# Kernel tuning notes

Hardware: AMD Instinct MI355X
Metric: run time of the kernel (lower is better)

The kernel has to match this reference:

```python
import jax, jax.numpy as jnp
import numpy as np

C = 512
B, H, W = 4, 64, 64
GROUPS = 32
EPS = 1e-6
SCALE = 1.0 / np.sqrt(C)


def setup_inputs() -> dict:
    key = jax.random.key(0)
    ks = jax.random.split(key, 3)
    x = jax.random.normal(ks[0], (B, C, H, W), dtype=jnp.float32)
    # conv weights: kaiming-ish small init for numerical sanity
    qkv_w = jax.random.normal(ks[1], (3 * C, C), dtype=jnp.float32) * (1.0 / np.sqrt(C))
    proj_w = jax.random.normal(ks[2], (C, C), dtype=jnp.float32) * (1.0 / np.sqrt(C))
    return {
        "x": x,
        "norm_w": jnp.ones((C,), jnp.float32),
        "norm_b": jnp.zeros((C,), jnp.float32),
        "qkv_w": qkv_w,
        "qkv_b": jnp.zeros((3 * C,), jnp.float32),
        "proj_w": proj_w,
        "proj_b": jnp.zeros((C,), jnp.float32),
    }


def reference(x, norm_w, norm_b, qkv_w, qkv_b, proj_w, proj_b):
    b, c, h, w = x.shape
    hw = h * w
    # GroupNorm(32, eps=1e-6, affine)
    xg = x.reshape(b, GROUPS, -1)                       # [B, G, (C/G)*H*W]
    mean = jnp.mean(xg, axis=-1, keepdims=True)
    var = jnp.var(xg, axis=-1, keepdims=True)
    xn = ((xg - mean) * jax.lax.rsqrt(var + EPS)).reshape(b, c, h, w)
    xn = xn * norm_w[:, None, None] + norm_b[:, None, None]
    # 1x1 conv qkv == channel matmul
    qkv = jnp.einsum('oc,bchw->bohw', qkv_w, xn) + qkv_b[:, None, None]
    q, k, v = jnp.split(qkv, 3, axis=1)                 # each [B, C, H, W]
    q = q.reshape(b, c, hw)                              # [B, C, HW]
    k = k.reshape(b, c, hw)
    v = v.reshape(b, c, hw)
    # attn[b, i, j] = softmax_j( q_i . k_j * scale )
    scores = jnp.einsum('bci,bcj->bij', q, k) * SCALE    # [B, HW, HW]
    attn = jax.nn.softmax(scores, axis=-1)
    # h[b, c, i] = sum_j v[b, c, j] * attn[b, i, j]
    hmap = jnp.einsum('bcj,bij->bci', v, attn).reshape(b, c, h, w)
    out = x + jnp.einsum('oc,bchw->bohw', proj_w, hmap) + proj_b[:, None, None]
    return out
```

## Files before the change

### kernel.cpp

```cpp
#include <hip/hip_runtime.h>
#include <hip/hip_fp8.h>
#include <cstdint>
#include <cmath>

#define B_   4
#define C_   512
#define HW_  4096
#define G_   32
#define CPG_ 16
#define EPS_ 1e-6f
#define SCALE_ 0.04419417382415922f
#define PSCALE_ 0.0625f


typedef __bf16 bf16_t;
typedef __bf16 bf16x8 __attribute__((ext_vector_type(8)));
typedef float  f32x4  __attribute__((ext_vector_type(4)));
typedef int    i32x4  __attribute__((ext_vector_type(4)));
typedef int    i32x8  __attribute__((ext_vector_type(8)));
typedef unsigned int u32;
typedef __hip_fp8_e4m3 fp8_t;

__device__ __forceinline__ void cp16(const void* g, void* l) {
  __builtin_amdgcn_global_load_lds((__attribute__((address_space(1))) u32*)(g),
                                   (__attribute__((address_space(3))) u32*)(l),
                                   16, 0, 0);
}

__device__ __forceinline__ void zero_acc(f32x4 acc[4][4]) {
  f32x4 z = {0.f, 0.f, 0.f, 0.f};
#pragma unroll
  for (int i = 0; i < 4; ++i)
#pragma unroll
    for (int j = 0; j < 4; ++j) acc[i][j] = z;
}

template <bool ROWSUM, int SA = 0x7F, int SB = 0x7F>
__device__ __forceinline__ void gemm_bt_mx(const unsigned char* __restrict__ A,
                                           const unsigned char* __restrict__ B,
                                           int K, int lda, int ldb,
                                           f32x4 acc[4][4], f32x4 accl[4]) {
  __shared__ __align__(16) unsigned char As[2][128 * 128];
  __shared__ __align__(16) unsigned char Bs[2][128 * 128];
  const int tid  = threadIdx.x;
  const int wave = tid >> 6;
  const int lane = tid & 63;
  const int wm = (wave >> 1) * 64;
  const int wn = (wave & 1) * 64;
  const int srow = lane >> 3;
  const int gch  = ((lane & 7) - srow) & 7;
  const unsigned char* gA = A + (size_t)(wave * 32 + srow) * lda + gch * 16;
  const unsigned char* gB = B + (size_t)(wave * 32 + srow) * ldb + gch * 16;
  const int lofs = wave * 32 * 128;
  const int fr = lane & 15;
  const int q  = lane >> 4;
  const int co0 = ((2 * q     + fr) & 7) * 16;
  const int co1 = ((2 * q + 1 + fr) & 7) * 16;
  const i32x8 vones = {0x38383838, 0x38383838, 0x38383838, 0x38383838,
                       0x38383838, 0x38383838, 0x38383838, 0x38383838};

  const int nT = K >> 7;
#pragma unroll
  for (int cc = 0; cc < 4; ++cc) {
    cp16(gA + (size_t)(cc * 8) * lda, &As[0][lofs + cc * 1024]);
    cp16(gB + (size_t)(cc * 8) * ldb, &Bs[0][lofs + cc * 1024]);
  }
  gA += 128; gB += 128;

#pragma unroll 1
  for (int t = 0; t < nT; ++t) {
    const int cur = t & 1;
    if (t + 1 < nT) {
#pragma unroll
      for (int cc = 0; cc < 4; ++cc) {
        cp16(gA + (size_t)(cc * 8) * lda, &As[cur ^ 1][lofs + cc * 1024]);
        cp16(gB + (size_t)(cc * 8) * ldb, &Bs[cur ^ 1][lofs + cc * 1024]);
      }
      gA += 128; gB += 128;
      asm volatile("s_waitcnt vmcnt(8)" ::: "memory");
    } else {
      asm volatile("s_waitcnt vmcnt(0)" ::: "memory");
    }
    __builtin_amdgcn_s_barrier();

    i32x8 a[4], b[4];
    const unsigned char* Ab = As[cur];
    const unsigned char* Bb = Bs[cur];
#pragma unroll
    for (int i = 0; i < 4; ++i) {
      const int ro = (wm + i * 16 + fr) * 128;
      i32x4 lo = *(const i32x4*)(Ab + ro + co0);
      i32x4 hi = *(const i32x4*)(Ab + ro + co1);
      a[i] = __builtin_shufflevector(lo, hi, 0, 1, 2, 3, 4, 5, 6, 7);
    }
#pragma unroll
    for (int j = 0; j < 4; ++j) {
      const int ro = (wn + j * 16 + fr) * 128;
      i32x4 lo = *(const i32x4*)(Bb + ro + co0);
      i32x4 hi = *(const i32x4*)(Bb + ro + co1);
      b[j] = __builtin_shufflevector(lo, hi, 0, 1, 2, 3, 4, 5, 6, 7);
    }
    __builtin_amdgcn_s_setprio(1);
#pragma unroll
    for (int i = 0; i < 4; ++i) {
#pragma unroll
      for (int j = 0; j < 4; ++j)
        acc[i][j] = __builtin_amdgcn_mfma_scale_f32_16x16x128_f8f6f4(
            a[i], b[j], acc[i][j], 0, 0, 0, SA, 0, SB);
      if (ROWSUM)
        accl[i] = __builtin_amdgcn_mfma_scale_f32_16x16x128_f8f6f4(
            a[i], vones, accl[i], 0, 0, 0, SA, 0, 0x7F);
    }
    __builtin_amdgcn_s_setprio(0);
    __builtin_amdgcn_s_barrier();
  }
}


__global__ void __launch_bounds__(256) cast_w_kernel(const float* __restrict__ qkv_w,
                                                     const float* __restrict__ proj_w,
                                                     fp8_t* __restrict__ wqkv8,
                                                     fp8_t* __restrict__ wproj8) {
  const int idx = blockIdx.x * 256 + threadIdx.x;
  const int t = idx * 4;
  const int nq = 1536 * 512;
  if (t < nq) {
    u32 dw = 0;
    dw = (u32)__builtin_amdgcn_cvt_pk_fp8_f32(qkv_w[t] * 16.f, qkv_w[t + 1] * 16.f, (int)dw, false);
    dw = (u32)__builtin_amdgcn_cvt_pk_fp8_f32(qkv_w[t + 2] * 16.f, qkv_w[t + 3] * 16.f, (int)dw, true);
    *(u32*)((unsigned char*)wqkv8 + t) = dw;
  } else {
    const int tt = t - nq;
    const int o = tt >> 9;
    const int p = tt & 511;
    float v[4];
#pragma unroll
    for (int e = 0; e < 4; ++e) {
      const int pe = p + e;
      const int off = pe & 63;
      const int c = (pe & ~63) + ((off & 3) << 4) + (off >> 2);
      v[e] = proj_w[(o << 9) + c] * 16.f;
    }
    u32 dw = 0;
    dw = (u32)__builtin_amdgcn_cvt_pk_fp8_f32(v[0], v[1], (int)dw, false);
    dw = (u32)__builtin_amdgcn_cvt_pk_fp8_f32(v[2], v[3], (int)dw, true);
    *(u32*)((unsigned char*)wproj8 + tt) = dw;
  }
}

__global__ void __launch_bounds__(256) gn_partial_kernel(const float* __restrict__ x,
                                                         float* __restrict__ stats) {
  __shared__ float rs[256], rss[256];
  const int bg = blockIdx.x >> 3;
  const int ch = blockIdx.x & 7;
  const float4* base = (const float4*)(x + (size_t)bg * (CPG_ * HW_)) +
                       (size_t)ch * (CPG_ * HW_ / 4 / 8);
  float s = 0.f, ss = 0.f;
  for (int i = threadIdx.x; i < CPG_ * HW_ / 4 / 8; i += 256) {
    float4 v = base[i];
    s  += v.x + v.y + v.z + v.w;
    ss += v.x * v.x + v.y * v.y + v.z * v.z + v.w * v.w;
  }
  rs[threadIdx.x] = s; rss[threadIdx.x] = ss;
  __syncthreads();
  for (int st = 128; st > 0; st >>= 1) {
    if ((int)threadIdx.x < st) {
      rs[threadIdx.x]  += rs[threadIdx.x + st];
      rss[threadIdx.x] += rss[threadIdx.x + st];
    }
    __syncthreads();
  }
  if (threadIdx.x == 0) {
    atomicAdd(&stats[bg * 2 + 0], rs[0]);
    atomicAdd(&stats[bg * 2 + 1], rss[0]);
  }
}

__global__ void __launch_bounds__(256) norm_tr_kernel(const float* __restrict__ x,
                                                      const float* __restrict__ stats,
                                                      const float* __restrict__ nw,
                                                      const float* __restrict__ nb,
                                                      fp8_t* __restrict__ xnT8) {
  __shared__ float tile[64][65];
  const int b  = blockIdx.z;
  const int i0 = blockIdx.x * 64;
  const int c0 = blockIdx.y * 64;
  const int tx = threadIdx.x & 63;
  const int ty = threadIdx.x >> 6;
  const int cbase = c0 + ty * 16;
  const int g = cbase >> 4;
  const float inv = 1.f / (float)(CPG_ * HW_);
  const float sum  = stats[(b * G_ + g) * 2 + 0];
  const float ssum = stats[(b * G_ + g) * 2 + 1];
  const float mean = sum * inv;
  const float rstd = rsqrtf(ssum * inv - mean * mean + EPS_);
#pragma unroll
  for (int r = 0; r < 16; ++r) {
    const int c = cbase + r;
    float v = x[((size_t)b * C_ + c) * HW_ + i0 + tx];
    tile[ty * 16 + r][tx] = (v - mean) * rstd * nw[c] + nb[c];
  }
  __syncthreads();
  const int il = threadIdx.x >> 2;
  const int q4 = threadIdx.x & 3;
#pragma unroll
  for (int m = 0; m < 4; ++m) {
    const int cq = q4 + m * 4;
    u32 dw = 0;
    dw = (u32)__builtin_amdgcn_cvt_pk_fp8_f32(tile[cq * 4 + 0][il], tile[cq * 4 + 1][il], (int)dw, false);
    dw = (u32)__builtin_amdgcn_cvt_pk_fp8_f32(tile[cq * 4 + 2][il], tile[cq * 4 + 3][il], (int)dw, true);
    *(u32*)((unsigned char*)xnT8 + ((size_t)b * HW_ + i0 + il) * C_ + c0 + cq * 4) = dw;
  }
}


__global__ void __launch_bounds__(256) qk_gemm_kernel(const fp8_t* __restrict__ xnT8,
                                                      const fp8_t* __restrict__ wqkv8,
                                                      const float* __restrict__ qkv_b,
                                                      fp8_t* __restrict__ QKt8) {
  const int b = blockIdx.z;
  f32x4 acc[4][4]; zero_acc(acc);
  const unsigned char* A  = (const unsigned char*)xnT8 + ((size_t)b * HW_ + blockIdx.y * 128) * C_;
  const unsigned char* Bp = (const unsigned char*)wqkv8 + (size_t)blockIdx.x * 128 * C_;
  gemm_bt_mx<false, 0x7F, 0x7B>(A, Bp, C_, C_, C_, acc, nullptr);
  const int lane = threadIdx.x & 63, wave = threadIdx.x >> 6;
  const int wm = (wave >> 1) * 64, wn = (wave & 1) * 64;
  const int fr = lane & 15, q = lane >> 4;
  const int r0 = blockIdx.y * 128 + wm + (q << 2);
  const int cb = blockIdx.x * 128 + wn;
  float bias[4];
#pragma unroll
  for (int j = 0; j < 4; ++j) bias[j] = qkv_b[cb + fr + j * 16];
#pragma unroll
  for (int i = 0; i < 4; ++i)
#pragma unroll
    for (int r = 0; r < 4; ++r) {
      const int row = r0 + i * 16 + r;
      u32 dw = 0;
      dw = (u32)__builtin_amdgcn_cvt_pk_fp8_f32(acc[i][0][r] + bias[0],
                                                acc[i][1][r] + bias[1], (int)dw, false);
      dw = (u32)__builtin_amdgcn_cvt_pk_fp8_f32(acc[i][2][r] + bias[2],
                                                acc[i][3][r] + bias[3], (int)dw, true);
      *(u32*)((unsigned char*)QKt8 + ((size_t)b * HW_ + row) * 1024 + cb + fr * 4) = dw;
    }
}

__global__ void __launch_bounds__(256) v_gemm_kernel(const fp8_t* __restrict__ wqkv8,
                                                     const fp8_t* __restrict__ xnT8,
                                                     const float* __restrict__ qkv_b,
                                                     fp8_t* __restrict__ V8) {
  const int b = blockIdx.z;
  f32x4 acc[4][4]; zero_acc(acc);
  const unsigned char* A  = (const unsigned char*)wqkv8 + (size_t)(1024 + blockIdx.y * 128) * C_;
  const unsigned char* Bp = (const unsigned char*)xnT8 + ((size_t)b * HW_ + blockIdx.x * 128) * C_;
  gemm_bt_mx<false, 0x7B, 0x7F>(A, Bp, C_, C_, C_, acc, nullptr);
  const int lane = threadIdx.x & 63, wave = threadIdx.x >> 6;
  const int wm = (wave >> 1) * 64, wn = (wave & 1) * 64;
  const int fr = lane & 15, q = lane >> 4;
  const int r0 = blockIdx.y * 128 + wm + (q << 2);
  const int cb = blockIdx.x * 128 + wn;
#pragma unroll
  for (int i = 0; i < 4; ++i)
#pragma unroll
    for (int r = 0; r < 4; ++r) {
      const int row = r0 + i * 16 + r;
      const float bias = qkv_b[1024 + row];
      u32 dw = 0;
      dw = (u32)__builtin_amdgcn_cvt_pk_fp8_f32(acc[i][0][r] + bias,
                                                acc[i][1][r] + bias, (int)dw, false);
      dw = (u32)__builtin_amdgcn_cvt_pk_fp8_f32(acc[i][2][r] + bias,
                                                acc[i][3][r] + bias, (int)dw, true);
      *(u32*)((unsigned char*)V8 + ((size_t)b * C_ + row) * HW_ + cb + fr * 4) = dw;
    }
}

__global__ void __launch_bounds__(256) sexp_gemm_kernel(const fp8_t* __restrict__ QKt8,
                                                        fp8_t* __restrict__ P8) {
  const int n   = blockIdx.x;
  const int xcd = n & 7;
  const int p   = n >> 3;
  const int xb  = p & 31;
  const int grp = xcd * 16 + (p >> 5);
  const int yb  = grp & 31;
  const int b   = grp >> 5;

  const unsigned char* QKtb = (const unsigned char*)QKt8 + (size_t)b * HW_ * 1024;
  fp8_t* Pb = P8 + (size_t)b * HW_ * HW_;
  f32x4 acc[4][4]; zero_acc(acc);
  const unsigned char* A  = QKtb + (size_t)yb * 128 * 1024;
  const unsigned char* Bp = QKtb + 512 + (size_t)xb * 128 * 1024;
  gemm_bt_mx<false>(A, Bp, 512, 1024, 1024, acc, nullptr);
  const int lane = threadIdx.x & 63, wave = threadIdx.x >> 6;
  const int wm = (wave >> 1) * 64, wn = (wave & 1) * 64;
  const int fr = lane & 15, q = lane >> 4;
  const int r0 = yb * 128 + wm + (q << 2);
  const int cb = xb * 128 + wn;
#pragma unroll
  for (int i = 0; i < 4; ++i)
#pragma unroll
    for (int r = 0; r < 4; ++r) {
      const int row = r0 + i * 16 + r;
      float e0 = __expf(acc[i][0][r] * SCALE_) * PSCALE_;
      float e1 = __expf(acc[i][1][r] * SCALE_) * PSCALE_;
      float e2 = __expf(acc[i][2][r] * SCALE_) * PSCALE_;
      float e3 = __expf(acc[i][3][r] * SCALE_) * PSCALE_;
      u32 dw = 0;
      dw = (u32)__builtin_amdgcn_cvt_pk_fp8_f32(e0, e1, (int)dw, false);
      dw = (u32)__builtin_amdgcn_cvt_pk_fp8_f32(e2, e3, (int)dw, true);
      *(u32*)((unsigned char*)Pb + (size_t)row * HW_ + cb + fr * 4) = dw;
    }
}

__global__ void __launch_bounds__(256) pv_gemm_kernel(const fp8_t* __restrict__ P8,
                                                      const fp8_t* __restrict__ V8,
                                                      fp8_t* __restrict__ hmT8) {
  const int n   = blockIdx.x;
  const int xcd = n & 7;
  const int p   = n >> 3;
  const int xb  = p & 3;
  const int grp = xcd * 16 + (p >> 2);
  const int yb  = grp & 31;
  const int b   = grp >> 5;

  const unsigned char* A  = (const unsigned char*)P8 + (size_t)b * HW_ * HW_ +
                            (size_t)yb * 128 * HW_;
  const unsigned char* Bp = (const unsigned char*)V8 + (size_t)b * C_ * HW_ +
                            (size_t)xb * 128 * HW_;
  fp8_t* hmTb = hmT8 + (size_t)b * HW_ * C_;

  f32x4 acc[4][4]; zero_acc(acc);
  f32x4 accl[4];
  {
    f32x4 z = {0.f, 0.f, 0.f, 0.f};
#pragma unroll
    for (int i = 0; i < 4; ++i) accl[i] = z;
  }
  gemm_bt_mx<true>(A, Bp, HW_, HW_, HW_, acc, accl);

  const int lane = threadIdx.x & 63, wave = threadIdx.x >> 6;
  const int wm = (wave >> 1) * 64, wn = (wave & 1) * 64;
  const int fr = lane & 15, q = lane >> 4;
  const int r0 = yb * 128 + wm + (q << 2);
  const int cb = xb * 128 + wn;
#pragma unroll
  for (int i = 0; i < 4; ++i)
#pragma unroll
    for (int r = 0; r < 4; ++r) {
      const int row = r0 + i * 16 + r;
      const float rl = 16.f / accl[i][r];
      u32 dw = 0;
      dw = (u32)__builtin_amdgcn_cvt_pk_fp8_f32(acc[i][0][r] * rl, acc[i][1][r] * rl, (int)dw, false);
      dw = (u32)__builtin_amdgcn_cvt_pk_fp8_f32(acc[i][2][r] * rl, acc[i][3][r] * rl, (int)dw, true);
      *(u32*)((unsigned char*)hmTb + (size_t)row * C_ + cb + fr * 4) = dw;
    }
}

__global__ void __launch_bounds__(256) proj_gemm_kernel(const fp8_t* __restrict__ wproj8,
                                                        const fp8_t* __restrict__ hmT8,
                                                        const float* __restrict__ proj_b,
                                                        const float* __restrict__ x,
                                                        float* __restrict__ out) {
  const int b = blockIdx.z;
  f32x4 acc[4][4]; zero_acc(acc);
  const unsigned char* A  = (const unsigned char*)wproj8 + (size_t)blockIdx.y * 128 * C_;
  const unsigned char* Bp = (const unsigned char*)hmT8 + ((size_t)b * HW_ + blockIdx.x * 128) * C_;
  gemm_bt_mx<false, 0x7B, 0x7B>(A, Bp, C_, C_, C_, acc, nullptr);
  const int lane = threadIdx.x & 63, wave = threadIdx.x >> 6;
  const int wm = (wave >> 1) * 64, wn = (wave & 1) * 64;
  const int r0 = blockIdx.y * 128 + wm + ((lane >> 4) << 2);
  const int c0 = blockIdx.x * 128 + wn + (lane & 15);
#pragma unroll
  for (int i = 0; i < 4; ++i)
#pragma unroll
    for (int r = 0; r < 4; ++r) {
      const int row = r0 + i * 16 + r;
      const float bias = proj_b[row];
#pragma unroll
      for (int j = 0; j < 4; ++j) {
        const int col = c0 + j * 16;
        const size_t idx = ((size_t)b * C_ + row) * HW_ + col;
        out[idx] = x[idx] + bias + acc[i][j][r];
      }
    }
}

extern "C" void kernel_launch(void* const* d_in, const int* in_sizes, int n_in,
                              void* d_out, int out_size, void* d_ws, size_t ws_size,
                              hipStream_t stream) {
  const float* x      = (const float*)d_in[0];
  const float* norm_w = (const float*)d_in[1];
  const float* norm_b = (const float*)d_in[2];
  const float* qkv_w  = (const float*)d_in[3];
  const float* qkv_b  = (const float*)d_in[4];
  const float* proj_w = (const float*)d_in[5];
  const float* proj_b = (const float*)d_in[6];
  float* out = (float*)d_out;

  char* ws = (char*)d_ws;
  size_t o = 0;
  fp8_t* wqkv8  = (fp8_t*)(ws + o); o += (size_t)1536 * 512;
  fp8_t* wproj8 = (fp8_t*)(ws + o); o += (size_t)512 * 512;
  float* stats  = (float*)(ws + o); o += 128 * 2 * 4;
  fp8_t* xnT8   = (fp8_t*)(ws + o); o += (size_t)B_ * HW_ * C_;
  fp8_t* QKt8   = (fp8_t*)(ws + o); o += (size_t)B_ * HW_ * 1024;
  fp8_t* V8     = (fp8_t*)(ws + o); o += (size_t)B_ * C_ * HW_;
  fp8_t* hmT8   = (fp8_t*)(ws + o); o += (size_t)B_ * HW_ * C_;
  fp8_t* P8     = (fp8_t*)(ws + o); o += (size_t)B_ * HW_ * HW_;

  cast_w_kernel<<<1024, 256, 0, stream>>>(qkv_w, proj_w, wqkv8, wproj8);
  hipMemsetAsync(stats, 0, 128 * 2 * sizeof(float), stream);
  gn_partial_kernel<<<1024, 256, 0, stream>>>(x, stats);
  norm_tr_kernel<<<dim3(HW_ / 64, C_ / 64, B_), 256, 0, stream>>>(x, stats, norm_w, norm_b, xnT8);
  qk_gemm_kernel<<<dim3(1024 / 128, HW_ / 128, B_), 256, 0, stream>>>(xnT8, wqkv8, qkv_b, QKt8);
  v_gemm_kernel<<<dim3(HW_ / 128, C_ / 128, B_), 256, 0, stream>>>(wqkv8, xnT8, qkv_b, V8);
  sexp_gemm_kernel<<<4096, 256, 0, stream>>>(QKt8, P8);
  pv_gemm_kernel<<<512, 256, 0, stream>>>(P8, V8, hmT8);
  proj_gemm_kernel<<<dim3(HW_ / 128, C_ / 128, B_), 256, 0, stream>>>(
      wproj8, hmT8, proj_b, x, out);
}
```

Measured before the change: 235.6 us.

## Merge prep and QK/V GEMM launches, use raw exp2 and rcp intrinsics

Folds the weight-cast and GroupNorm-stats kernels into one launch, and the QK and V projection GEMMs into one 1536-block launch that picks its branch by block index. This cuts launch count and lets the two independent phases share the GPU instead of running back to back. The softmax exponent now uses a raw v_exp_f32 with scale and bias folded into one FMA. The final normalisation uses a hardware reciprocal instead of a divide. LDS buffers move from the shared GEMM helper into each kernel, which is needed so the fused kernel can use a single allocation. These are modest savings and carry slight accuracy changes from the approximate exp and reciprocal.

```diff
diff --git a/kernel.cpp b/kernel.cpp
--- a/kernel.cpp
+++ b/kernel.cpp
@@ -11,6 +11,7 @@
 #define EPS_ 1e-6f
 #define SCALE_ 0.04419417382415922f
 #define PSCALE_ 0.0625f
+#define SEXPC_ 0.063758715306f
 
 
 typedef __bf16 bf16_t;
@@ -27,6 +28,12 @@
                                    16, 0, 0);
 }
 
+__device__ __forceinline__ float fexp2(float x) {
+  float r;
+  asm("v_exp_f32 %0, %1\n\ts_nop 1" : "=v"(r) : "v"(x));
+  return r;
+}
+
 __device__ __forceinline__ void zero_acc(f32x4 acc[4][4]) {
   f32x4 z = {0.f, 0.f, 0.f, 0.f};
 #pragma unroll
@@ -39,9 +46,8 @@
 __device__ __forceinline__ void gemm_bt_mx(const unsigned char* __restrict__ A,
                                            const unsigned char* __restrict__ B,
                                            int K, int lda, int ldb,
-                                           f32x4 acc[4][4], f32x4 accl[4]) {
-  __shared__ __align__(16) unsigned char As[2][128 * 128];
-  __shared__ __align__(16) unsigned char Bs[2][128 * 128];
+                                           f32x4 acc[4][4], f32x4 accl[4],
+                                           unsigned char* AsB, unsigned char* BsB) {
   const int tid  = threadIdx.x;
   const int wave = tid >> 6;
   const int lane = tid & 63;
@@ -62,8 +68,8 @@
   const int nT = K >> 7;
 #pragma unroll
   for (int cc = 0; cc < 4; ++cc) {
-    cp16(gA + (size_t)(cc * 8) * lda, &As[0][lofs + cc * 1024]);
-    cp16(gB + (size_t)(cc * 8) * ldb, &Bs[0][lofs + cc * 1024]);
+    cp16(gA + (size_t)(cc * 8) * lda, AsB + lofs + cc * 1024);
+    cp16(gB + (size_t)(cc * 8) * ldb, BsB + lofs + cc * 1024);
   }
   gA += 128; gB += 128;
 
@@ -73,8 +79,8 @@
     if (t + 1 < nT) {
 #pragma unroll
       for (int cc = 0; cc < 4; ++cc) {
-        cp16(gA + (size_t)(cc * 8) * lda, &As[cur ^ 1][lofs + cc * 1024]);
-        cp16(gB + (size_t)(cc * 8) * ldb, &Bs[cur ^ 1][lofs + cc * 1024]);
+        cp16(gA + (size_t)(cc * 8) * lda, AsB + (cur ^ 1) * 16384 + lofs + cc * 1024);
+        cp16(gB + (size_t)(cc * 8) * ldb, BsB + (cur ^ 1) * 16384 + lofs + cc * 1024);
       }
       gA += 128; gB += 128;
       asm volatile("s_waitcnt vmcnt(8)" ::: "memory");
@@ -84,8 +90,8 @@
     __builtin_amdgcn_s_barrier();
 
     i32x8 a[4], b[4];
-    const unsigned char* Ab = As[cur];
-    const unsigned char* Bb = Bs[cur];
+    const unsigned char* Ab = AsB + cur * 16384;
+    const unsigned char* Bb = BsB + cur * 16384;
 #pragma unroll
     for (int i = 0; i < 4; ++i) {
       const int ro = (wm + i * 16 + fr) * 128;
@@ -117,62 +123,64 @@
 }
 
 
-__global__ void __launch_bounds__(256) cast_w_kernel(const float* __restrict__ qkv_w,
-                                                     const float* __restrict__ proj_w,
-                                                     fp8_t* __restrict__ wqkv8,
-                                                     fp8_t* __restrict__ wproj8) {
-  const int idx = blockIdx.x * 256 + threadIdx.x;
-  const int t = idx * 4;
-  const int nq = 1536 * 512;
-  if (t < nq) {
-    u32 dw = 0;
-    dw = (u32)__builtin_amdgcn_cvt_pk_fp8_f32(qkv_w[t] * 16.f, qkv_w[t + 1] * 16.f, (int)dw, false);
-    dw = (u32)__builtin_amdgcn_cvt_pk_fp8_f32(qkv_w[t + 2] * 16.f, qkv_w[t + 3] * 16.f, (int)dw, true);
-    *(u32*)((unsigned char*)wqkv8 + t) = dw;
+__global__ void __launch_bounds__(256) prep_kernel(const float* __restrict__ x,
+                                                   float* __restrict__ stats,
+                                                   const float* __restrict__ qkv_w,
+                                                   const float* __restrict__ proj_w,
+                                                   fp8_t* __restrict__ wqkv8,
+                                                   fp8_t* __restrict__ wproj8) {
+  __shared__ float rs[256], rss[256];
+  const int n = blockIdx.x;
+  if (n < 1024) {
+    const int bg = n >> 3;
+    const int ch = n & 7;
+    const float4* base = (const float4*)(x + (size_t)bg * (CPG_ * HW_)) +
+                         (size_t)ch * (CPG_ * HW_ / 4 / 8);
+    float s = 0.f, ss = 0.f;
+    for (int i = threadIdx.x; i < CPG_ * HW_ / 4 / 8; i += 256) {
+      float4 v = base[i];
+      s  += v.x + v.y + v.z + v.w;
+      ss += v.x * v.x + v.y * v.y + v.z * v.z + v.w * v.w;
+    }
+    rs[threadIdx.x] = s; rss[threadIdx.x] = ss;
+    __syncthreads();
+    for (int st = 128; st > 0; st >>= 1) {
+      if ((int)threadIdx.x < st) {
+        rs[threadIdx.x]  += rs[threadIdx.x + st];
+        rss[threadIdx.x] += rss[threadIdx.x + st];
+      }
+      __syncthreads();
+    }
+    if (threadIdx.x == 0) {
+      atomicAdd(&stats[bg * 2 + 0], rs[0]);
+      atomicAdd(&stats[bg * 2 + 1], rss[0]);
+    }
   } else {
-    const int tt = t - nq;
-    const int o = tt >> 9;
-    const int p = tt & 511;
-    float v[4];
-#pragma unroll
-    for (int e = 0; e < 4; ++e) {
-      const int pe = p + e;
-      const int off = pe & 63;
-      const int c = (pe & ~63) + ((off & 3) << 4) + (off >> 2);
-      v[e] = proj_w[(o << 9) + c] * 16.f;
-    }
-    u32 dw = 0;
-    dw = (u32)__builtin_amdgcn_cvt_pk_fp8_f32(v[0], v[1], (int)dw, false);
-    dw = (u32)__builtin_amdgcn_cvt_pk_fp8_f32(v[2], v[3], (int)dw, true);
-    *(u32*)((unsigned char*)wproj8 + tt) = dw;
-  }
-}
-
-__global__ void __launch_bounds__(256) gn_partial_kernel(const float* __restrict__ x,
-                                                         float* __restrict__ stats) {
-  __shared__ float rs[256], rss[256];
-  const int bg = blockIdx.x >> 3;
-  const int ch = blockIdx.x & 7;
-  const float4* base = (const float4*)(x + (size_t)bg * (CPG_ * HW_)) +
-                       (size_t)ch * (CPG_ * HW_ / 4 / 8);
-  float s = 0.f, ss = 0.f;
-  for (int i = threadIdx.x; i < CPG_ * HW_ / 4 / 8; i += 256) {
-    float4 v = base[i];
-    s  += v.x + v.y + v.z + v.w;
-    ss += v.x * v.x + v.y * v.y + v.z * v.z + v.w * v.w;
-  }
-  rs[threadIdx.x] = s; rss[threadIdx.x] = ss;
-  __syncthreads();
-  for (int st = 128; st > 0; st >>= 1) {
-    if ((int)threadIdx.x < st) {
-      rs[threadIdx.x]  += rs[threadIdx.x + st];
-      rss[threadIdx.x] += rss[threadIdx.x + st];
-    }
-    __syncthreads();
-  }
-  if (threadIdx.x == 0) {
-    atomicAdd(&stats[bg * 2 + 0], rs[0]);
-    atomicAdd(&stats[bg * 2 + 1], rss[0]);
+    const int idx = (n - 1024) * 256 + threadIdx.x;
+    const int t = idx * 4;
+    const int nq = 1536 * 512;
+    if (t < nq) {
+      u32 dw = 0;
+      dw = (u32)__builtin_amdgcn_cvt_pk_fp8_f32(qkv_w[t] * 16.f, qkv_w[t + 1] * 16.f, (int)dw, false);
+      dw = (u32)__builtin_amdgcn_cvt_pk_fp8_f32(qkv_w[t + 2] * 16.f, qkv_w[t + 3] * 16.f, (int)dw, true);
+      *(u32*)((unsigned char*)wqkv8 + t) = dw;
+    } else {
+      const int tt = t - nq;
+      const int o = tt >> 9;
+      const int p = tt & 511;
+      float v[4];
+#pragma unroll
+      for (int e = 0; e < 4; ++e) {
+        const int pe = p + e;
+        const int off = pe & 63;
+        const int c = (pe & ~63) + ((off & 3) << 4) + (off >> 2);
+        v[e] = proj_w[(o << 9) + c] * 16.f;
+      }
+      u32 dw = 0;
+      dw = (u32)__builtin_amdgcn_cvt_pk_fp8_f32(v[0], v[1], (int)dw, false);
+      dw = (u32)__builtin_amdgcn_cvt_pk_fp8_f32(v[2], v[3], (int)dw, true);
+      *(u32*)((unsigned char*)wproj8 + tt) = dw;
+    }
   }
 }
 
@@ -214,68 +222,69 @@
 }
 
 
-__global__ void __launch_bounds__(256) qk_gemm_kernel(const fp8_t* __restrict__ xnT8,
-                                                      const fp8_t* __restrict__ wqkv8,
-                                                      const float* __restrict__ qkv_b,
-                                                      fp8_t* __restrict__ QKt8) {
-  const int b = blockIdx.z;
-  f32x4 acc[4][4]; zero_acc(acc);
-  const unsigned char* A  = (const unsigned char*)xnT8 + ((size_t)b * HW_ + blockIdx.y * 128) * C_;
-  const unsigned char* Bp = (const unsigned char*)wqkv8 + (size_t)blockIdx.x * 128 * C_;
-  gemm_bt_mx<false, 0x7F, 0x7B>(A, Bp, C_, C_, C_, acc, nullptr);
+__global__ void __launch_bounds__(256) qkv_gemm_kernel(const fp8_t* __restrict__ xnT8,
+                                                       const fp8_t* __restrict__ wqkv8,
+                                                       const float* __restrict__ qkv_b,
+                                                       fp8_t* __restrict__ QKt8,
+                                                       fp8_t* __restrict__ V8) {
+  __shared__ __align__(16) unsigned char As[2 * 16384];
+  __shared__ __align__(16) unsigned char Bs[2 * 16384];
+  const int n = blockIdx.x;
   const int lane = threadIdx.x & 63, wave = threadIdx.x >> 6;
   const int wm = (wave >> 1) * 64, wn = (wave & 1) * 64;
   const int fr = lane & 15, q = lane >> 4;
-  const int r0 = blockIdx.y * 128 + wm + (q << 2);
-  const int cb = blockIdx.x * 128 + wn;
-  float bias[4];
-#pragma unroll
-  for (int j = 0; j < 4; ++j) bias[j] = qkv_b[cb + fr + j * 16];
-#pragma unroll
-  for (int i = 0; i < 4; ++i)
-#pragma unroll
-    for (int r = 0; r < 4; ++r) {
-      const int row = r0 + i * 16 + r;
-      u32 dw = 0;
-      dw = (u32)__builtin_amdgcn_cvt_pk_fp8_f32(acc[i][0][r] + bias[0],
-                                                acc[i][1][r] + bias[1], (int)dw, false);
-      dw = (u32)__builtin_amdgcn_cvt_pk_fp8_f32(acc[i][2][r] + bias[2],
-                                                acc[i][3][r] + bias[3], (int)dw, true);
-      *(u32*)((unsigned char*)QKt8 + ((size_t)b * HW_ + row) * 1024 + cb + fr * 4) = dw;
-    }
-}
-
-__global__ void __launch_bounds__(256) v_gemm_kernel(const fp8_t* __restrict__ wqkv8,
-                                                     const fp8_t* __restrict__ xnT8,
-                                                     const float* __restrict__ qkv_b,
-                                                     fp8_t* __restrict__ V8) {
-  const int b = blockIdx.z;
   f32x4 acc[4][4]; zero_acc(acc);
-  const unsigned char* A  = (const unsigned char*)wqkv8 + (size_t)(1024 + blockIdx.y * 128) * C_;
-  const unsigned char* Bp = (const unsigned char*)xnT8 + ((size_t)b * HW_ + blockIdx.x * 128) * C_;
-  gemm_bt_mx<false, 0x7B, 0x7F>(A, Bp, C_, C_, C_, acc, nullptr);
-  const int lane = threadIdx.x & 63, wave = threadIdx.x >> 6;
-  const int wm = (wave >> 1) * 64, wn = (wave & 1) * 64;
-  const int fr = lane & 15, q = lane >> 4;
-  const int r0 = blockIdx.y * 128 + wm + (q << 2);
-  const int cb = blockIdx.x * 128 + wn;
-#pragma unroll
-  for (int i = 0; i < 4; ++i)
-#pragma unroll
-    for (int r = 0; r < 4; ++r) {
-      const int row = r0 + i * 16 + r;
-      const float bias = qkv_b[1024 + row];
-      u32 dw = 0;
-      dw = (u32)__builtin_amdgcn_cvt_pk_fp8_f32(acc[i][0][r] + bias,
-                                                acc[i][1][r] + bias, (int)dw, false);
-      dw = (u32)__builtin_amdgcn_cvt_pk_fp8_f32(acc[i][2][r] + bias,
-                                                acc[i][3][r] + bias, (int)dw, true);
-      *(u32*)((unsigned char*)V8 + ((size_t)b * C_ + row) * HW_ + cb + fr * 4) = dw;
-    }
+
+  if (n < 1024) {
+    const int xb = n & 7, yb = (n >> 3) & 31, b = n >> 8;
+    const unsigned char* A  = (const unsigned char*)xnT8 + ((size_t)b * HW_ + yb * 128) * C_;
+    const unsigned char* Bp = (const unsigned char*)wqkv8 + (size_t)xb * 128 * C_;
+    gemm_bt_mx<false, 0x7F, 0x7B>(A, Bp, C_, C_, C_, acc, nullptr, As, Bs);
+    const int r0 = yb * 128 + wm + (q << 2);
+    const int cb = xb * 128 + wn;
+    float bias[4];
+#pragma unroll
+    for (int j = 0; j < 4; ++j) bias[j] = qkv_b[cb + fr + j * 16];
+#pragma unroll
+    for (int i = 0; i < 4; ++i)
+#pragma unroll
+      for (int r = 0; r < 4; ++r) {
+        const int row = r0 + i * 16 + r;
+        u32 dw = 0;
+        dw = (u32)__builtin_amdgcn_cvt_pk_fp8_f32(acc[i][0][r] + bias[0],
+                                                  acc[i][1][r] + bias[1], (int)dw, false);
+        dw = (u32)__builtin_amdgcn_cvt_pk_fp8_f32(acc[i][2][r] + bias[2],
+                                                  acc[i][3][r] + bias[3], (int)dw, true);
+        *(u32*)((unsigned char*)QKt8 + ((size_t)b * HW_ + row) * 1024 + cb + fr * 4) = dw;
+      }
+  } else {
+    const int m = n - 1024;
+    const int xb = m & 31, yb = (m >> 5) & 3, b = m >> 7;
+    const unsigned char* A  = (const unsigned char*)wqkv8 + (size_t)(1024 + yb * 128) * C_;
+    const unsigned char* Bp = (const unsigned char*)xnT8 + ((size_t)b * HW_ + xb * 128) * C_;
+    gemm_bt_mx<false, 0x7B, 0x7F>(A, Bp, C_, C_, C_, acc, nullptr, As, Bs);
+    const int r0 = yb * 128 + wm + (q << 2);
+    const int cb = xb * 128 + wn;
+#pragma unroll
+    for (int i = 0; i < 4; ++i)
+#pragma unroll
+      for (int r = 0; r < 4; ++r) {
+        const int row = r0 + i * 16 + r;
+        const float bias = qkv_b[1024 + row];
+        u32 dw = 0;
+        dw = (u32)__builtin_amdgcn_cvt_pk_fp8_f32(acc[i][0][r] + bias,
+                                                  acc[i][1][r] + bias, (int)dw, false);
+        dw = (u32)__builtin_amdgcn_cvt_pk_fp8_f32(acc[i][2][r] + bias,
+                                                  acc[i][3][r] + bias, (int)dw, true);
+        *(u32*)((unsigned char*)V8 + ((size_t)b * C_ + row) * HW_ + cb + fr * 4) = dw;
+      }
+  }
 }
 
 __global__ void __launch_bounds__(256) sexp_gemm_kernel(const fp8_t* __restrict__ QKt8,
                                                         fp8_t* __restrict__ P8) {
+  __shared__ __align__(16) unsigned char As[2 * 16384];
+  __shared__ __align__(16) unsigned char Bs[2 * 16384];
   const int n   = blockIdx.x;
   const int xcd = n & 7;
   const int p   = n >> 3;
@@ -289,7 +298,7 @@
   f32x4 acc[4][4]; zero_acc(acc);
   const unsigned char* A  = QKtb + (size_t)yb * 128 * 1024;
   const unsigned char* Bp = QKtb + 512 + (size_t)xb * 128 * 1024;
-  gemm_bt_mx<false>(A, Bp, 512, 1024, 1024, acc, nullptr);
+  gemm_bt_mx<false>(A, Bp, 512, 1024, 1024, acc, nullptr, As, Bs);
   const int lane = threadIdx.x & 63, wave = threadIdx.x >> 6;
   const int wm = (wave >> 1) * 64, wn = (wave & 1) * 64;
   const int fr = lane & 15, q = lane >> 4;
@@ -300,10 +309,10 @@
 #pragma unroll
     for (int r = 0; r < 4; ++r) {
       const int row = r0 + i * 16 + r;
-      float e0 = __expf(acc[i][0][r] * SCALE_) * PSCALE_;
-      float e1 = __expf(acc[i][1][r] * SCALE_) * PSCALE_;
-      float e2 = __expf(acc[i][2][r] * SCALE_) * PSCALE_;
-      float e3 = __expf(acc[i][3][r] * SCALE_) * PSCALE_;
+      float e0 = fexp2(fmaf(acc[i][0][r], SEXPC_, -4.0f));
+      float e1 = fexp2(fmaf(acc[i][1][r], SEXPC_, -4.0f));
+      float e2 = fexp2(fmaf(acc[i][2][r], SEXPC_, -4.0f));
+      float e3 = fexp2(fmaf(acc[i][3][r], SEXPC_, -4.0f));
       u32 dw = 0;
       dw = (u32)__builtin_amdgcn_cvt_pk_fp8_f32(e0, e1, (int)dw, false);
       dw = (u32)__builtin_amdgcn_cvt_pk_fp8_f32(e2, e3, (int)dw, true);
@@ -314,6 +323,8 @@
 __global__ void __launch_bounds__(256) pv_gemm_kernel(const fp8_t* __restrict__ P8,
                                                       const fp8_t* __restrict__ V8,
                                                       fp8_t* __restrict__ hmT8) {
+  __shared__ __align__(16) unsigned char As[2 * 16384];
+  __shared__ __align__(16) unsigned char Bs[2 * 16384];
   const int n   = blockIdx.x;
   const int xcd = n & 7;
   const int p   = n >> 3;
@@ -335,7 +346,7 @@
 #pragma unroll
     for (int i = 0; i < 4; ++i) accl[i] = z;
   }
-  gemm_bt_mx<true>(A, Bp, HW_, HW_, HW_, acc, accl);
+  gemm_bt_mx<true>(A, Bp, HW_, HW_, HW_, acc, accl, As, Bs);
 
   const int lane = threadIdx.x & 63, wave = threadIdx.x >> 6;
   const int wm = (wave >> 1) * 64, wn = (wave & 1) * 64;
@@ -347,7 +358,7 @@
 #pragma unroll
     for (int r = 0; r < 4; ++r) {
       const int row = r0 + i * 16 + r;
-      const float rl = 16.f / accl[i][r];
+      const float rl = 16.f * __builtin_amdgcn_rcpf(accl[i][r]);
       u32 dw = 0;
       dw = (u32)__builtin_amdgcn_cvt_pk_fp8_f32(acc[i][0][r] * rl, acc[i][1][r] * rl, (int)dw, false);
       dw = (u32)__builtin_amdgcn_cvt_pk_fp8_f32(acc[i][2][r] * rl, acc[i][3][r] * rl, (int)dw, true);
@@ -360,11 +371,13 @@
                                                         const float* __restrict__ proj_b,
                                                         const float* __restrict__ x,
                                                         float* __restrict__ out) {
+  __shared__ __align__(16) unsigned char As[2 * 16384];
+  __shared__ __align__(16) unsigned char Bs[2 * 16384];
   const int b = blockIdx.z;
   f32x4 acc[4][4]; zero_acc(acc);
   const unsigned char* A  = (const unsigned char*)wproj8 + (size_t)blockIdx.y * 128 * C_;
   const unsigned char* Bp = (const unsigned char*)hmT8 + ((size_t)b * HW_ + blockIdx.x * 128) * C_;
-  gemm_bt_mx<false, 0x7B, 0x7B>(A, Bp, C_, C_, C_, acc, nullptr);
+  gemm_bt_mx<false, 0x7B, 0x7B>(A, Bp, C_, C_, C_, acc, nullptr, As, Bs);
   const int lane = threadIdx.x & 63, wave = threadIdx.x >> 6;
   const int wm = (wave >> 1) * 64, wn = (wave & 1) * 64;
   const int r0 = blockIdx.y * 128 + wm + ((lane >> 4) << 2);
@@ -407,12 +420,10 @@
   fp8_t* hmT8   = (fp8_t*)(ws + o); o += (size_t)B_ * HW_ * C_;
   fp8_t* P8     = (fp8_t*)(ws + o); o += (size_t)B_ * HW_ * HW_;
 
-  cast_w_kernel<<<1024, 256, 0, stream>>>(qkv_w, proj_w, wqkv8, wproj8);
   hipMemsetAsync(stats, 0, 128 * 2 * sizeof(float), stream);
-  gn_partial_kernel<<<1024, 256, 0, stream>>>(x, stats);
+  prep_kernel<<<2048, 256, 0, stream>>>(x, stats, qkv_w, proj_w, wqkv8, wproj8);
   norm_tr_kernel<<<dim3(HW_ / 64, C_ / 64, B_), 256, 0, stream>>>(x, stats, norm_w, norm_b, xnT8);
-  qk_gemm_kernel<<<dim3(1024 / 128, HW_ / 128, B_), 256, 0, stream>>>(xnT8, wqkv8, qkv_b, QKt8);
-  v_gemm_kernel<<<dim3(HW_ / 128, C_ / 128, B_), 256, 0, stream>>>(wqkv8, xnT8, qkv_b, V8);
+  qkv_gemm_kernel<<<1536, 256, 0, stream>>>(xnT8, wqkv8, qkv_b, QKt8, V8);
   sexp_gemm_kernel<<<4096, 256, 0, stream>>>(QKt8, P8);
   pv_gemm_kernel<<<512, 256, 0, stream>>>(P8, V8, hmT8);
   proj_gemm_kernel<<<dim3(HW_ / 128, C_ / 128, B_), 256, 0, stream>>>(
```

After: 229.7 us. 1.03x faster.
